# Optimization experiments

Measured on AMD Instinct MI355X. Metric: run time of the kernel, lower is better.

## Reference

```python
import jax, jax.numpy as jnp
import numpy as np

NHEAD = 16


def setup_inputs() -> dict:
    key = jax.random.key(0)
    ks = jax.random.split(key, 9)
    d = 1024
    scale = 0.03  # keep projected q,k in a sane range (like trained weights)
    return {
        "x": jax.random.normal(ks[0], (4, 4096, d), jnp.float32),
        "wq": jax.random.normal(ks[1], (d, d), jnp.float32) * scale,
        "bq": jax.random.normal(ks[2], (d,), jnp.float32) * scale,
        "wk": jax.random.normal(ks[3], (d, d), jnp.float32) * scale,
        "bk": jax.random.normal(ks[4], (d,), jnp.float32) * scale,
        "wv": jax.random.normal(ks[5], (d, d), jnp.float32) * scale,
        "bv": jax.random.normal(ks[6], (d,), jnp.float32) * scale,
        "wo": jax.random.normal(ks[7], (d, d), jnp.float32) * scale,
        "bo": jax.random.normal(ks[8], (d,), jnp.float32) * scale,
        "window_size": 128,
    }


def reference(x, wq, bq, wk, bk, wv, bv, wo, bo, window_size):
    B, S, D = x.shape
    H = NHEAD
    Dh = D // H
    w = int(window_size)

    def proj(wm, b):
        # [B,S,D] -> [B,H,S,Dh]
        return (x @ wm.T + b).reshape(B, S, H, Dh).transpose(0, 2, 1, 3)

    q = proj(wq, bq)
    k = proj(wk, bk)
    v = proj(wv, bv)

    # Pad K/V along seq so offset slices are static-size [B,H,S,Dh].
    Kp = jnp.pad(k, ((0, 0), (0, 0), (w, w), (0, 0)))
    Vp = jnp.pad(v, ((0, 0), (0, 0), (w, w), (0, 0)))
    pos = jnp.arange(S)
    inv_sqrt = np.float32(1.0 / np.sqrt(Dh))

    # Faithful to the Triton kernel: a sequential scan over window offsets with a
    # RUNNING max but NO rescaling of the accumulators (the kernel's exact math).
    def step(carry, t):
        m, o_acc, t_acc = carry
        kj = jax.lax.dynamic_slice_in_dim(Kp, t, S, axis=2)  # key at offset t-w
        vj = jax.lax.dynamic_slice_in_dim(Vp, t, S, axis=2)
        s = jnp.einsum("bhsd,bhsd->bhs", q, kj) * inv_sqrt
        j = pos + t - w
        valid = (j >= 0) & (j < S)  # [S], broadcasts over [B,H,S]
        m_new = jnp.where(valid, jnp.maximum(m, s), m)
        p = jnp.exp(jnp.where(valid, s - m_new, -jnp.inf))  # 0 where invalid
        return (m_new, o_acc + p[..., None] * vj, t_acc + p), None

    init = (
        jnp.full((B, H, S), -jnp.inf, dtype=x.dtype),
        jnp.zeros((B, H, S, Dh), dtype=x.dtype),
        jnp.zeros((B, H, S), dtype=x.dtype),
    )
    (m, o_acc, t_acc), _ = jax.lax.scan(step, init, jnp.arange(2 * w + 1))
    o = o_acc / t_acc[..., None]  # [B,H,S,Dh]
    out = o.transpose(0, 2, 1, 3).reshape(B, S, D)
    return out @ wo.T + bo
```

## Files before the change

### kernel.cpp

```cpp
#include <hip/hip_runtime.h>
#include <math.h>

#define S_LEN  4096
#define BATCH  4
#define DMODEL 1024
#define NHEADS 16
#define DHEAD  64
#define WIN    128

typedef _Float16 half8   __attribute__((ext_vector_type(8)));
typedef _Float16 half4_t __attribute__((ext_vector_type(4)));
typedef float    floatx4 __attribute__((ext_vector_type(4)));

__device__ __forceinline__ void gload16(const void* g, void* l) {
    __builtin_amdgcn_global_load_lds(
        (const __attribute__((address_space(1))) void*)g,
        (__attribute__((address_space(3))) void*)l, 16, 0, 0);
}

__global__ __launch_bounds__(256)
void cvt_f32_f16(const float4* __restrict__ in, half4_t* __restrict__ out, int n4) {
    for (int i = blockIdx.x * blockDim.x + threadIdx.x; i < n4;
         i += gridDim.x * blockDim.x) {
        const float4 a = in[i];
        half4_t h;
        h[0] = (_Float16)a.x; h[1] = (_Float16)a.y;
        h[2] = (_Float16)a.z; h[3] = (_Float16)a.w;
        out[i] = h;
    }
}

__global__ __launch_bounds__(256)
void cvt4_f32_f16(const float4* __restrict__ w0, const float4* __restrict__ w1,
                  const float4* __restrict__ w2, const float4* __restrict__ w3,
                  half4_t* __restrict__ o0, half4_t* __restrict__ o1,
                  half4_t* __restrict__ o2, half4_t* __restrict__ o3, int n4) {
    const float4* in  = blockIdx.y == 0 ? w0 : (blockIdx.y == 1 ? w1 : (blockIdx.y == 2 ? w2 : w3));
    half4_t*      out = blockIdx.y == 0 ? o0 : (blockIdx.y == 1 ? o1 : (blockIdx.y == 2 ? o2 : o3));
    for (int i = blockIdx.x * blockDim.x + threadIdx.x; i < n4;
         i += gridDim.x * blockDim.x) {
        const float4 a = in[i];
        half4_t h;
        h[0] = (_Float16)a.x; h[1] = (_Float16)a.y;
        h[2] = (_Float16)a.z; h[3] = (_Float16)a.w;
        out[i] = h;
    }
}

template<int MODE, int NTN>
__global__ __launch_bounds__(512)
void gemm8p(const _Float16* __restrict__ A, const _Float16* __restrict__ W,
            const float* __restrict__ B0, const float* __restrict__ B1,
            const float* __restrict__ B2, void* __restrict__ out_base)
{
    constexpr int K  = DMODEL;
    constexpr int nt = K / 64;
    const int bid  = blockIdx.x;
    const int nwg8 = (64 * NTN) >> 3;
    const int swz  = (bid & 7) * nwg8 + (bid >> 3);
    const int i0   = (swz / NTN) * 256;
    const int n0   = (swz % NTN) * 256;

    __shared__ _Float16 As[4][128 * 64];
    __shared__ _Float16 Bs[4][128 * 64];

    const int tid  = threadIdx.x;
    const int lane = tid & 63;
    const int wid  = tid >> 6;
    const int wr   = wid >> 2;
    const int wc   = wid & 3;
    const int fr   = lane & 15;
    const int fh   = lane >> 4;
    const int sw   = fr & 7;
    const int ok0  = ((fh) ^ sw) * 8;
    const int ok1  = ((4 + fh) ^ sw) * 8;
    const int arow = (wr * 16 + fr) * 64;
    const int brow = (wc * 16 + fr) * 64;

    const int srow  = tid >> 3;
    const int ssw   = ((tid & 7) ^ (srow & 7)) << 3;

    auto stA = [&](int t, int h) {
        _Float16* dst = &As[((t & 1) << 1) | h][(size_t)tid * 8];
        const _Float16* src = A + (size_t)(i0 + h * 128 + srow) * K + t * 64 + ssw;
        gload16(src, dst);
        gload16(src + (size_t)64 * K, dst + 4096);
    };
    auto stB = [&](int t, int h) {
        _Float16* dst = &Bs[((t & 1) << 1) | h][(size_t)tid * 8];
        const _Float16* src = W + (size_t)(n0 + h * 128 + srow) * K + t * 64 + ssw;
        gload16(src, dst);
        gload16(src + (size_t)64 * K, dst + 4096);
    };

    floatx4 acc[8][4];
    #pragma unroll
    for (int mi = 0; mi < 8; ++mi)
        #pragma unroll
        for (int ni = 0; ni < 4; ++ni) acc[mi][ni] = (floatx4)0.f;

    stB(0, 0); stA(0, 1);
    stA(0, 0); stB(0, 1);
    stB(1, 0); stA(1, 1);
    asm volatile("s_waitcnt vmcnt(4)" ::: "memory");
    __builtin_amdgcn_s_barrier();

    half8 a[4][2], b[2][2];

#define RD_A(HALF)                                                           \
    _Pragma("unroll")                                                        \
    for (int mi = 0; mi < 4; ++mi) {                                         \
        a[mi][0] = *(const half8*)&As[d2 | HALF][arow + mi * 2048 + ok0];    \
        a[mi][1] = *(const half8*)&As[d2 | HALF][arow + mi * 2048 + ok1];    \
    }
#define RD_B(HALF)                                                           \
    _Pragma("unroll")                                                        \
    for (int ni = 0; ni < 2; ++ni) {                                         \
        b[ni][0] = *(const half8*)&Bs[d2 | HALF][brow + ni * 4096 + ok0];    \
        b[ni][1] = *(const half8*)&Bs[d2 | HALF][brow + ni * 4096 + ok1];    \
    }
#define MFMA_QUAD(MB, NB)                                                    \
    __builtin_amdgcn_s_setprio(1);                                           \
    _Pragma("unroll")                                                        \
    for (int kc = 0; kc < 2; ++kc)                                           \
        _Pragma("unroll")                                                    \
        for (int mi = 0; mi < 4; ++mi)                                       \
            _Pragma("unroll")                                                \
            for (int ni = 0; ni < 2; ++ni)                                   \
                acc[MB + mi][NB + ni] = __builtin_amdgcn_mfma_f32_16x16x32_f16( \
                    a[mi][kc], b[ni][kc], acc[MB + mi][NB + ni], 0, 0, 0);   \
    __builtin_amdgcn_s_setprio(0);
#define WAIT_LDS                                                             \
    asm volatile("s_waitcnt lgkmcnt(0)" ::: "memory");                       \
    __builtin_amdgcn_sched_barrier(0);

    for (int t = 0; t < nt; ++t) {
        const int d2 = (t & 1) << 1;
        RD_A(0); RD_B(0);
        if (t + 1 < nt) stA(t + 1, 0);
        __builtin_amdgcn_s_barrier();
        WAIT_LDS;
        MFMA_QUAD(0, 0);
        __builtin_amdgcn_s_barrier();
        RD_A(1);
        if (t + 1 < nt) stB(t + 1, 1);
        __builtin_amdgcn_s_barrier();
        WAIT_LDS;
        MFMA_QUAD(4, 0);
        __builtin_amdgcn_s_barrier();
        RD_B(1);
        if (t + 2 < nt) stB(t + 2, 0);
        __builtin_amdgcn_s_barrier();
        WAIT_LDS;
        MFMA_QUAD(4, 2);
        __builtin_amdgcn_s_barrier();
        RD_A(0);
        if (t + 2 < nt) stA(t + 2, 1);
        __builtin_amdgcn_s_barrier();
        WAIT_LDS;
        MFMA_QUAD(0, 2);
        if (t + 2 < nt) {
            asm volatile("s_waitcnt vmcnt(4)" ::: "memory");
        } else if (t + 1 < nt) {
            asm volatile("s_waitcnt vmcnt(0)" ::: "memory");
        }
        __builtin_amdgcn_s_barrier();
    }
#undef RD_A
#undef RD_B
#undef MFMA_QUAD
#undef WAIT_LDS

    const int z  = (MODE == 0) ? (n0 >> 10) : 0;
    const float* bz = (MODE == 1) ? B0 : (z == 0 ? B0 : (z == 1 ? B1 : B2));

    #pragma unroll
    for (int ni = 0; ni < 4; ++ni) {
        const int gc   = n0 + ni * 64 + wc * 16 + fr;
        const int gcol = gc & (DMODEL - 1);
        const float bv = bz[gcol];
        #pragma unroll
        for (int mi = 0; mi < 8; ++mi) {
            const int gr = i0 + mi * 32 + wr * 16 + fh * 4;
            const floatx4 v = acc[mi][ni];
            if (MODE == 0) {
                _Float16* outh = (_Float16*)out_base
                               + (size_t)z * ((size_t)16384 * DMODEL);
                const int bb = gr >> 12;
                const int sp = gr & (S_LEN - 1);
                const int hh = gcol >> 6;
                const int dh = gcol & 63;
                if (z < 2) {
                    #pragma unroll
                    for (int r = 0; r < 4; ++r)
                        outh[((((size_t)(bb * NHEADS + hh)) * S_LEN + sp + r) << 6) + dh] =
                            (_Float16)(v[r] + bv);
                } else {
                    half4_t hv;
                    hv[0] = (_Float16)(v[0] + bv); hv[1] = (_Float16)(v[1] + bv);
                    hv[2] = (_Float16)(v[2] + bv); hv[3] = (_Float16)(v[3] + bv);
                    *(half4_t*)&outh[(((size_t)(bb * NHEADS + hh)) * DHEAD + dh) * S_LEN + sp] = hv;
                }
            } else {
                float* out = (float*)out_base;
                #pragma unroll
                for (int r = 0; r < 4; ++r)
                    out[(size_t)(gr + r) * DMODEL + gcol] = v[r] + bv;
            }
        }
    }
}

__global__ __launch_bounds__(256)
void attn_mfma(const _Float16* __restrict__ qh_, const _Float16* __restrict__ kh_,
               const _Float16* __restrict__ vth_, _Float16* __restrict__ o)
{
    __shared__ __align__(16) _Float16 Qs[64 * 64];
    __shared__ __align__(16) _Float16 Ks[64 * 64];
    __shared__ __align__(16) _Float16 Vt[64 * 64];
    __shared__ __align__(16) float    SP[64 * 68];
    __shared__ __align__(16) _Float16 P16[64 * 64];
    __shared__ float CM[64 * 4];
    __shared__ float TSs[64 * 4];
    __shared__ float Mq[64];
    __shared__ float Tq[64];

    const int tid   = threadIdx.x;
    const int lane  = tid & 63;
    const int w     = tid >> 6;
    const int qbase = blockIdx.x * 64;
    const int head  = blockIdx.y, b = blockIdx.z;
    const size_t bh = (size_t)(b * NHEADS + head);

    const _Float16* qg = qh_  + bh * (size_t)(S_LEN * DHEAD);
    const _Float16* kg = kh_  + bh * (size_t)(S_LEN * DHEAD);
    const _Float16* vg = vth_ + bh * (size_t)(DHEAD * S_LEN);

    const int fr = lane & 15;
    const int fh = lane >> 4;

    #pragma unroll
    for (int rep = 0; rep < 2; ++rep) {
        const int c = tid + 256 * rep;
        const int row = c >> 3, sll = c & 7;
        gload16(qg + (size_t)(qbase + row) * 64 + (size_t)((sll ^ (row & 7)) * 8),
                Qs + (size_t)c * 8);
    }
    if (tid < 64) { Mq[tid] = -INFINITY; Tq[tid] = 0.f; }

    floatx4 Oacc[4];
    #pragma unroll
    for (int ni = 0; ni < 4; ++ni) Oacc[ni] = (floatx4)0.f;

    for (int c = 0; c < 5; ++c) {
        const int jlo = qbase - WIN + c * 64;
        if (jlo < 0 || jlo >= S_LEN) continue;
        const int base_rel = jlo - qbase + WIN;

        __syncthreads();

        #pragma unroll
        for (int rep = 0; rep < 2; ++rep) {
            const int cc = tid + 256 * rep;
            const int row = cc >> 3, sll = cc & 7;
            gload16(kg + (size_t)(jlo + row) * 64 + (size_t)((sll ^ (row & 7)) * 8),
                    Ks + (size_t)cc * 8);
            gload16(vg + (size_t)row * S_LEN + jlo + (size_t)((sll ^ (row & 7)) * 8),
                    Vt + (size_t)cc * 8);
        }
        __syncthreads();

        {
            floatx4 acc[4];
            #pragma unroll
            for (int ni = 0; ni < 4; ++ni) acc[ni] = (floatx4)0.f;
            half8 a[2];
            #pragma unroll
            for (int kc = 0; kc < 2; ++kc) {
                const int row = 16 * w + fr;
                a[kc] = *(const half8*)&Qs[row * 64 + ((fh + 4 * kc) ^ (row & 7)) * 8];
            }
            #pragma unroll
            for (int ni = 0; ni < 4; ++ni)
                #pragma unroll
                for (int kc = 0; kc < 2; ++kc) {
                    const int tr = 16 * ni + fr;
                    half8 bf = *(const half8*)&Ks[tr * 64 + ((fh + 4 * kc) ^ (tr & 7)) * 8];
                    acc[ni] = __builtin_amdgcn_mfma_f32_16x16x32_f16(a[kc], bf, acc[ni], 0, 0, 0);
                }
            #pragma unroll
            for (int ni = 0; ni < 4; ++ni)
                #pragma unroll
                for (int r = 0; r < 4; ++r)
                    SP[(16 * w + 4 * fh + r) * 68 + fr + 16 * ni] = acc[ni][r] * 0.125f;
        }
        __syncthreads();

        const int sq = lane;
        float sv[16], run[16];
        {
            float m_run = -INFINITY;
            #pragma unroll
            for (int u = 0; u < 4; ++u) {
                const float4 s4 = *(const float4*)&SP[sq * 68 + w * 16 + 4 * u];
                const float se[4] = {s4.x, s4.y, s4.z, s4.w};
                #pragma unroll
                for (int e = 0; e < 4; ++e) {
                    const int i = 4 * u + e;
                    const int rel = base_rel + 16 * w + i - sq;
                    const bool valid = (rel >= 0) && (rel <= 2 * WIN);
                    const float s = valid ? se[e] : -INFINITY;
                    sv[i] = s;
                    m_run = fmaxf(m_run, s);
                    run[i] = m_run;
                }
            }
            CM[sq * 4 + w] = m_run;
        }
        __syncthreads();

        {
            float pre = Mq[sq];
            if (w > 0) pre = fmaxf(pre, CM[sq * 4 + 0]);
            if (w > 1) pre = fmaxf(pre, CM[sq * 4 + 1]);
            if (w > 2) pre = fmaxf(pre, CM[sq * 4 + 2]);
            float tl = 0.f;
            _Float16 pf[16];
            #pragma unroll
            for (int i = 0; i < 16; ++i) {
                const float wv = fmaxf(pre, run[i]);
                const float p = (sv[i] != -INFINITY) ? __expf(sv[i] - wv) : 0.f;
                tl += p;
                pf[i] = (_Float16)p;
            }
            TSs[sq * 4 + w] = tl;
            #pragma unroll
            for (int u = 0; u < 2; ++u) {
                half8 h8;
                #pragma unroll
                for (int e = 0; e < 8; ++e) h8[e] = pf[8 * u + e];
                *(half8*)&P16[sq * 64 + ((2 * w + u) ^ (sq & 7)) * 8] = h8;
            }
        }
        __syncthreads();

        if (tid < 64) {
            const float mm = fmaxf(fmaxf(CM[tid * 4 + 0], CM[tid * 4 + 1]),
                                   fmaxf(CM[tid * 4 + 2], CM[tid * 4 + 3]));
            Mq[tid] = fmaxf(Mq[tid], mm);
            Tq[tid] += TSs[tid * 4 + 0] + TSs[tid * 4 + 1] + TSs[tid * 4 + 2] + TSs[tid * 4 + 3];
        }

        {
            half8 pa[2];
            #pragma unroll
            for (int kc = 0; kc < 2; ++kc) {
                const int row = 16 * w + fr;
                pa[kc] = *(const half8*)&P16[row * 64 + ((fh + 4 * kc) ^ (row & 7)) * 8];
            }
            #pragma unroll
            for (int ni = 0; ni < 4; ++ni)
                #pragma unroll
                for (int kc = 0; kc < 2; ++kc) {
                    const int dr = 16 * ni + fr;
                    half8 bf = *(const half8*)&Vt[dr * 64 + ((fh + 4 * kc) ^ (dr & 7)) * 8];
                    Oacc[ni] = __builtin_amdgcn_mfma_f32_16x16x32_f16(pa[kc], bf, Oacc[ni], 0, 0, 0);
                }
        }
    }

    __syncthreads();

    #pragma unroll
    for (int ni = 0; ni < 4; ++ni)
        #pragma unroll
        for (int r = 0; r < 4; ++r) {
            const int q  = 16 * w + 4 * fh + r;
            const float inv = 1.0f / Tq[q];
            o[((size_t)(b * S_LEN + qbase + q) * NHEADS + head) * DHEAD + fr + 16 * ni] =
                (_Float16)(Oacc[ni][r] * inv);
        }
}

extern "C" void kernel_launch(void* const* d_in, const int* in_sizes, int n_in,
                              void* d_out, int out_size, void* d_ws, size_t ws_size,
                              hipStream_t stream) {
    const float* x  = (const float*)d_in[0];
    const float* wq = (const float*)d_in[1];
    const float* bq = (const float*)d_in[2];
    const float* wk = (const float*)d_in[3];
    const float* bk = (const float*)d_in[4];
    const float* wv = (const float*)d_in[5];
    const float* bv = (const float*)d_in[6];
    const float* wo = (const float*)d_in[7];
    const float* bo = (const float*)d_in[8];

    const size_t BUF = (size_t)BATCH * S_LEN * DMODEL;
    _Float16* xh  = (_Float16*)d_ws;
    _Float16* qh  = xh + BUF;
    _Float16* kh  = qh + BUF;
    _Float16* vth = kh + BUF;
    _Float16* oh  = vth + BUF;
    _Float16* wqh = oh + BUF;
    _Float16* wkh = wqh + DMODEL * DMODEL;
    _Float16* wvh = wkh + DMODEL * DMODEL;
    _Float16* woh = wvh + DMODEL * DMODEL;

    cvt_f32_f16<<<2048, 256, 0, stream>>>((const float4*)x, (half4_t*)xh, (int)(BUF / 4));
    cvt4_f32_f16<<<dim3(256, 4), 256, 0, stream>>>(
        (const float4*)wq, (const float4*)wk, (const float4*)wv, (const float4*)wo,
        (half4_t*)wqh, (half4_t*)wkh, (half4_t*)wvh, (half4_t*)woh,
        DMODEL * DMODEL / 4);

    gemm8p<0, 12><<<64 * 12, 512, 0, stream>>>(xh, wqh, bq, bk, bv, (void*)qh);

    dim3 gattn(S_LEN / 64, NHEADS, BATCH);
    attn_mfma<<<gattn, 256, 0, stream>>>(qh, kh, vth, oh);

    gemm8p<1, 4><<<64 * 4, 512, 0, stream>>>(oh, woh, bo, bo, bo, d_out);
}
```

Before: 269.6 us.

## Restructure GEMM main loop to overlap LDS fragment reads with MFMA

The GEMM k-loop is rescheduled so each phase issues the LDS reads for the next operand fragments while the current MFMA quad runs. Separate lo and hi register sets for the A and B fragments make this possible. Each phase now needs one barrier instead of two, and the global-to-LDS prefetch goes two tiles ahead with a deeper vmcnt wait. The aim is to hide LDS latency and cut barrier stalls, at the cost of more VGPRs and a more fragile ordering of buffer reuse.

```diff
diff --git a/kernel.cpp b/kernel.cpp
--- a/kernel.cpp
+++ b/kernel.cpp
@@ -71,27 +71,17 @@
     const int wc   = wid & 3;
     const int fr   = lane & 15;
     const int fh   = lane >> 4;
-    const int sw   = fr & 7;
-    const int ok0  = ((fh) ^ sw) * 8;
-    const int ok1  = ((4 + fh) ^ sw) * 8;
+    const int sw8  = fr & 7;
+    const int ok0  = ((fh) ^ sw8) * 8;
+    const int ok1  = ((4 + fh) ^ sw8) * 8;
     const int arow = (wr * 16 + fr) * 64;
     const int brow = (wc * 16 + fr) * 64;
 
-    const int srow  = tid >> 3;
-    const int ssw   = ((tid & 7) ^ (srow & 7)) << 3;
-
-    auto stA = [&](int t, int h) {
-        _Float16* dst = &As[((t & 1) << 1) | h][(size_t)tid * 8];
-        const _Float16* src = A + (size_t)(i0 + h * 128 + srow) * K + t * 64 + ssw;
-        gload16(src, dst);
-        gload16(src + (size_t)64 * K, dst + 4096);
-    };
-    auto stB = [&](int t, int h) {
-        _Float16* dst = &Bs[((t & 1) << 1) | h][(size_t)tid * 8];
-        const _Float16* src = W + (size_t)(n0 + h * 128 + srow) * K + t * 64 + ssw;
-        gload16(src, dst);
-        gload16(src + (size_t)64 * K, dst + 4096);
-    };
+    const int srow = tid >> 3;
+    const int ssw  = ((tid & 7) ^ (srow & 7)) << 3;
+    const _Float16* baseA = A + (size_t)(i0 + srow) * K + ssw;
+    const _Float16* baseB = W + (size_t)(n0 + srow) * K + ssw;
+    const int ldso = tid * 8;
 
     floatx4 acc[8][4];
     #pragma unroll
@@ -99,27 +89,35 @@
         #pragma unroll
         for (int ni = 0; ni < 4; ++ni) acc[mi][ni] = (floatx4)0.f;
 
-    stB(0, 0); stA(0, 1);
-    stA(0, 0); stB(0, 1);
-    stB(1, 0); stA(1, 1);
-    asm volatile("s_waitcnt vmcnt(4)" ::: "memory");
-    __builtin_amdgcn_s_barrier();
-
-    half8 a[4][2], b[2][2];
-
-#define RD_A(HALF)                                                           \
+    half8 a_lo[4][2], a_hi[4][2], b_lo[2][2], b_hi[2][2];
+
+#define ST_A(TT, H)                                                          \
+    do {                                                                     \
+        _Float16* d_ = &As[(((TT) & 1) << 1) | (H)][ldso];                   \
+        const _Float16* s_ = baseA + (size_t)((H) * 128) * K + (TT) * 64;    \
+        gload16(s_, d_);                                                     \
+        gload16(s_ + (size_t)64 * K, d_ + 4096);                             \
+    } while (0)
+#define ST_B(TT, H)                                                          \
+    do {                                                                     \
+        _Float16* d_ = &Bs[(((TT) & 1) << 1) | (H)][ldso];                   \
+        const _Float16* s_ = baseB + (size_t)((H) * 128) * K + (TT) * 64;    \
+        gload16(s_, d_);                                                     \
+        gload16(s_ + (size_t)64 * K, d_ + 4096);                             \
+    } while (0)
+#define RD_A(DST, DB, H)                                                     \
     _Pragma("unroll")                                                        \
     for (int mi = 0; mi < 4; ++mi) {                                         \
-        a[mi][0] = *(const half8*)&As[d2 | HALF][arow + mi * 2048 + ok0];    \
-        a[mi][1] = *(const half8*)&As[d2 | HALF][arow + mi * 2048 + ok1];    \
-    }
-#define RD_B(HALF)                                                           \
+        DST[mi][0] = *(const half8*)&As[(DB) | (H)][arow + mi * 2048 + ok0]; \
+        DST[mi][1] = *(const half8*)&As[(DB) | (H)][arow + mi * 2048 + ok1]; \
+    }
+#define RD_B(DST, DB, H)                                                     \
     _Pragma("unroll")                                                        \
     for (int ni = 0; ni < 2; ++ni) {                                         \
-        b[ni][0] = *(const half8*)&Bs[d2 | HALF][brow + ni * 4096 + ok0];    \
-        b[ni][1] = *(const half8*)&Bs[d2 | HALF][brow + ni * 4096 + ok1];    \
-    }
-#define MFMA_QUAD(MB, NB)                                                    \
+        DST[ni][0] = *(const half8*)&Bs[(DB) | (H)][brow + ni * 4096 + ok0]; \
+        DST[ni][1] = *(const half8*)&Bs[(DB) | (H)][brow + ni * 4096 + ok1]; \
+    }
+#define MFMA16(MB, NB, AA, BB)                                               \
     __builtin_amdgcn_s_setprio(1);                                           \
     _Pragma("unroll")                                                        \
     for (int kc = 0; kc < 2; ++kc)                                           \
@@ -128,48 +126,57 @@
             _Pragma("unroll")                                                \
             for (int ni = 0; ni < 2; ++ni)                                   \
                 acc[MB + mi][NB + ni] = __builtin_amdgcn_mfma_f32_16x16x32_f16( \
-                    a[mi][kc], b[ni][kc], acc[MB + mi][NB + ni], 0, 0, 0);   \
+                    AA[mi][kc], BB[ni][kc], acc[MB + mi][NB + ni], 0, 0, 0); \
     __builtin_amdgcn_s_setprio(0);
-#define WAIT_LDS                                                             \
+#define PHEND                                                                \
     asm volatile("s_waitcnt lgkmcnt(0)" ::: "memory");                       \
+    __builtin_amdgcn_sched_barrier(0);                                       \
+    __builtin_amdgcn_s_barrier();
+
+    ST_A(0, 0); ST_B(0, 0); ST_B(0, 1); ST_A(0, 1);
+    ST_A(1, 0); ST_B(1, 1); ST_A(1, 1); ST_B(1, 0);
+    asm volatile("s_waitcnt vmcnt(8)" ::: "memory");
+    __builtin_amdgcn_sched_barrier(0);
+    __builtin_amdgcn_s_barrier();
+    RD_A(a_lo, 0, 0); RD_B(b_lo, 0, 0);
+    asm volatile("s_waitcnt lgkmcnt(0)" ::: "memory");
     __builtin_amdgcn_sched_barrier(0);
 
     for (int t = 0; t < nt; ++t) {
         const int d2 = (t & 1) << 1;
-        RD_A(0); RD_B(0);
-        if (t + 1 < nt) stA(t + 1, 0);
-        __builtin_amdgcn_s_barrier();
-        WAIT_LDS;
-        MFMA_QUAD(0, 0);
-        __builtin_amdgcn_s_barrier();
-        RD_A(1);
-        if (t + 1 < nt) stB(t + 1, 1);
-        __builtin_amdgcn_s_barrier();
-        WAIT_LDS;
-        MFMA_QUAD(4, 0);
-        __builtin_amdgcn_s_barrier();
-        RD_B(1);
-        if (t + 2 < nt) stB(t + 2, 0);
-        __builtin_amdgcn_s_barrier();
-        WAIT_LDS;
-        MFMA_QUAD(4, 2);
-        __builtin_amdgcn_s_barrier();
-        RD_A(0);
-        if (t + 2 < nt) stA(t + 2, 1);
-        __builtin_amdgcn_s_barrier();
-        WAIT_LDS;
-        MFMA_QUAD(0, 2);
-        if (t + 2 < nt) {
-            asm volatile("s_waitcnt vmcnt(4)" ::: "memory");
+        const bool st = (t + 2) < nt;
+        RD_B(b_hi, d2, 1);
+        MFMA16(0, 0, a_lo, b_lo);
+        PHEND;
+        RD_A(a_hi, d2, 1);
+        if (st) { ST_B(t + 2, 1); ST_A(t + 2, 0); }
+        MFMA16(0, 2, a_lo, b_hi);
+        PHEND;
+        if (st) ST_A(t + 2, 1);
+        MFMA16(4, 2, a_hi, b_hi);
+        PHEND;
+        if (st) ST_B(t + 2, 0);
+        MFMA16(4, 0, a_hi, b_lo);
+        if (st) {
+            asm volatile("s_waitcnt vmcnt(8)" ::: "memory");
         } else if (t + 1 < nt) {
             asm volatile("s_waitcnt vmcnt(0)" ::: "memory");
         }
+        __builtin_amdgcn_sched_barrier(0);
         __builtin_amdgcn_s_barrier();
-    }
+        if (t + 1 < nt) {
+            const int dn = ((t + 1) & 1) << 1;
+            RD_A(a_lo, dn, 0); RD_B(b_lo, dn, 0);
+            asm volatile("s_waitcnt lgkmcnt(0)" ::: "memory");
+            __builtin_amdgcn_sched_barrier(0);
+        }
+    }
+#undef ST_A
+#undef ST_B
 #undef RD_A
 #undef RD_B
-#undef MFMA_QUAD
-#undef WAIT_LDS
+#undef MFMA16
+#undef PHEND
 
     const int z  = (MODE == 0) ? (n0 >> 10) : 0;
     const float* bz = (MODE == 1) ? B0 : (z == 0 ? B0 : (z == 1 ? B1 : B2));
```

Result: faster. 254.1 us (-5.7%).
